# Optimization experiments

Hardware: AMD Instinct MI355X
Metric: run time of the kernel (lower is better)

Reference implementation:

```python
import jax, jax.numpy as jnp
import numpy as np

B, Q, E, NH, L, P = 8, 1024, 256, 8, 4, 4
DH = E // NH
SHAPES = np.array([[128, 128], [64, 64], [32, 32], [16, 16]], dtype=np.int64)
STARTS = np.concatenate([[0], np.cumsum(SHAPES.prod(1))[:-1]]).astype(np.int64)
S_TOTAL = int(SHAPES.prod(1).sum())
EPS = 1e-5


def setup_inputs() -> dict:
    key = jax.random.key(0)
    ks = iter(jax.random.split(key, 40))
    def rn(shp, s=0.02):
        return jax.random.normal(next(ks), shp, jnp.float32) * s
    return {
        "tgt": rn((B, Q, E), 1.0),
        "query_pos": rn((B, Q, E), 1.0),
        "reference_points": jax.random.uniform(next(ks), (B, Q, L, 2), jnp.float32),
        "src": rn((B, S_TOTAL, E), 1.0),
        "spatial_shapes": jnp.asarray(SHAPES),
        "level_start_index": jnp.asarray(STARTS),
        "in_proj_w": rn((3 * E, E)), "in_proj_b": jnp.zeros((3 * E,), jnp.float32),
        "out_proj_w": rn((E, E)), "out_proj_b": jnp.zeros((E,), jnp.float32),
        "norm1_g": jnp.ones((E,), jnp.float32), "norm1_b": jnp.zeros((E,), jnp.float32),
        "off_w": rn((NH * L * P * 2, E)), "off_b": rn((NH * L * P * 2,), 0.5),
        "aw_w": rn((NH * L * P, E)), "aw_b": jnp.zeros((NH * L * P,), jnp.float32),
        "vp_w": rn((E, E)), "vp_b": jnp.zeros((E,), jnp.float32),
        "op_w": rn((E, E)), "op_b": jnp.zeros((E,), jnp.float32),
        "norm2_g": jnp.ones((E,), jnp.float32), "norm2_b": jnp.zeros((E,), jnp.float32),
        "w1": rn((4 * E, E)), "b1": jnp.zeros((4 * E,), jnp.float32),
        "w2": rn((E, 4 * E)), "b2": jnp.zeros((E,), jnp.float32),
        "norm3_g": jnp.ones((E,), jnp.float32), "norm3_b": jnp.zeros((E,), jnp.float32),
    }


def _ln(x, g, b):
    mu = x.mean(-1, keepdims=True)
    var = ((x - mu) ** 2).mean(-1, keepdims=True)
    return (x - mu) * jax.lax.rsqrt(var + EPS) * g + b


def _bilinear(v, loc, Hl, Wl):
    # v: [B,NH,S_l,DH], loc in [0,1]: [B,NH,Q,P,2] -> [B,NH,Q,P,DH]
    # matches torch grid_sample(align_corners=False, padding='zeros')
    x = loc[..., 0] * Wl - 0.5
    y = loc[..., 1] * Hl - 0.5
    x0 = jnp.floor(x)
    y0 = jnp.floor(y)
    wx = (x - x0)[..., None]
    wy = (y - y0)[..., None]
    def g(yi, xi):
        valid = ((xi >= 0) & (xi <= Wl - 1) & (yi >= 0) & (yi <= Hl - 1)).astype(v.dtype)
        idx = (jnp.clip(yi, 0, Hl - 1) * Wl + jnp.clip(xi, 0, Wl - 1)).astype(jnp.int32)
        out = jnp.take_along_axis(v, idx.reshape(B, NH, Q * P, 1), axis=2)
        return out.reshape(B, NH, Q, P, DH) * valid[..., None]
    v00 = g(y0, x0); v01 = g(y0, x0 + 1.0)
    v10 = g(y0 + 1.0, x0); v11 = g(y0 + 1.0, x0 + 1.0)
    return (v00 * (1 - wy) * (1 - wx) + v01 * (1 - wy) * wx
            + v10 * wy * (1 - wx) + v11 * wy * wx)


def _forward(tgt, query_pos, reference_points, src,
             in_proj_w, in_proj_b, out_proj_w, out_proj_b, norm1_g, norm1_b,
             off_w, off_b, aw_w, aw_b, vp_w, vp_b, op_w, op_b,
             norm2_g, norm2_b, w1, b1, w2, b2, norm3_g, norm3_b,
             spatial_shapes, level_start_index):
    shp = np.asarray(spatial_shapes)
    starts = np.asarray(level_start_index)
    # ---- self-attention (q = k = tgt + pos, v = tgt) ----
    qk = tgt + query_pos
    wq, wk, wv = jnp.split(in_proj_w, 3, axis=0)
    bq, bk, bv = jnp.split(in_proj_b, 3, axis=0)
    q = (qk @ wq.T + bq).reshape(B, Q, NH, DH)
    k = (qk @ wk.T + bk).reshape(B, Q, NH, DH)
    v = (tgt @ wv.T + bv).reshape(B, Q, NH, DH)
    scores = jnp.einsum("bqhd,bkhd->bhqk", q, k) / jnp.sqrt(jnp.float32(DH))
    attn = jax.nn.softmax(scores, axis=-1)
    ctx = jnp.einsum("bhqk,bkhd->bqhd", attn, v).reshape(B, Q, E)
    tgt = _ln(tgt + (ctx @ out_proj_w.T + out_proj_b), norm1_g, norm1_b)
    # ---- MSDA cross-attention ----
    query = tgt + query_pos
    value = (src @ vp_w.T + vp_b).reshape(B, S_TOTAL, NH, DH).transpose(0, 2, 1, 3)  # [B,NH,S,DH]
    off = (query @ off_w.T + off_b).reshape(B, Q, NH, L, P, 2)
    aw = jax.nn.softmax((query @ aw_w.T + aw_b).reshape(B, Q, NH, L * P), -1)
    aw = aw.reshape(B, Q, NH, L, P)
    normalizer = jnp.asarray(shp[:, ::-1].copy(), jnp.float32)  # [L,2] = (W,H)
    loc = reference_points[:, :, None, :, None, :] + off / normalizer[None, None, None, :, None, :]
    loc = jnp.transpose(loc, (0, 2, 1, 3, 4, 5))  # [B,NH,Q,L,P,2]
    awt = jnp.transpose(aw, (0, 2, 1, 3, 4))      # [B,NH,Q,L,P]
    out = jnp.zeros((B, NH, Q, DH), jnp.float32)
    for l in range(L):
        Hl, Wl = int(shp[l, 0]), int(shp[l, 1])
        s0 = int(starts[l])
        vl = value[:, :, s0:s0 + Hl * Wl]
        samp = _bilinear(vl, loc[:, :, :, l], Hl, Wl)         # [B,NH,Q,P,DH]
        out = out + (samp * awt[:, :, :, l, :, None]).sum(3)
    ca = out.transpose(0, 2, 1, 3).reshape(B, Q, E) @ op_w.T + op_b
    tgt = _ln(tgt + ca, norm2_g, norm2_b)
    # ---- FFN ----
    h = jax.nn.relu(tgt @ w1.T + b1) @ w2.T + b2
    return _ln(tgt + h, norm3_g, norm3_b)


def reference(tgt, query_pos, reference_points, src, spatial_shapes, level_start_index,
              in_proj_w, in_proj_b, out_proj_w, out_proj_b, norm1_g, norm1_b,
              off_w, off_b, aw_w, aw_b, vp_w, vp_b, op_w, op_b,
              norm2_g, norm2_b, w1, b1, w2, b2, norm3_g, norm3_b):
    return _forward(tgt, query_pos, reference_points, src,
                    in_proj_w, in_proj_b, out_proj_w, out_proj_b, norm1_g, norm1_b,
                    off_w, off_b, aw_w, aw_b, vp_w, vp_b, op_w, op_b,
                    norm2_g, norm2_b, w1, b1, w2, b2, norm3_g, norm3_b,
                    spatial_shapes, level_start_index)
```

## Files before the change

kernel.cpp:

```cpp
#include <hip/hip_runtime.h>
#include <hip/hip_bf16.h>
#include <math.h>

typedef __hip_bfloat16 bf16;
typedef unsigned short ushort_t;

#define BQ 8
#define QLEN 1024
#define EMB 256
#define NHD 8
#define NLVL 4
#define NPT 4
#define DHD 32
#define STOT 21760

typedef short s8v __attribute__((ext_vector_type(8)));
typedef float f4v __attribute__((ext_vector_type(4)));

__device__ __forceinline__ float b2f(bf16 x) { return __bfloat162float(x); }

__device__ __forceinline__ float ldin(const void* p, int bf, size_t i) {
    return bf ? __bfloat162float(((const bf16*)p)[i]) : ((const float*)p)[i];
}

__device__ __forceinline__ float bfraw(unsigned u) {
    union { unsigned i; float f; } c; c.i = u << 16; return c.f;
}

__device__ __forceinline__ unsigned short f2us(float x) {
    bf16 h = __float2bfloat16(x);
    unsigned short u;
    __builtin_memcpy(&u, &h, 2);
    return u;
}

__device__ __forceinline__ void ld4(const void* p, int bf, size_t i, float* o) {
    if (bf) {
        const uint2 u = *(const uint2*)((const ushort_t*)p + i);
        o[0] = bfraw(u.x & 0xffffu); o[1] = bfraw(u.x >> 16);
        o[2] = bfraw(u.y & 0xffffu); o[3] = bfraw(u.y >> 16);
    } else {
        const float4 f = *(const float4*)((const float*)p + i);
        o[0] = f.x; o[1] = f.y; o[2] = f.z; o[3] = f.w;
    }
}

typedef const __attribute__((address_space(1))) unsigned int* gas1_u32;
typedef __attribute__((address_space(3))) unsigned int* las3_u32;
__device__ __forceinline__ void gload_lds16(const void* g, void* l) {
    __builtin_amdgcn_global_load_lds((gas1_u32)g, (las3_u32)l, 16, 0, 0);
}

__global__ void detect_dtype(const unsigned* __restrict__ n1g, int* __restrict__ flag) {
    if (threadIdx.x == 0) flag[0] = (n1g[0] == 0x3F800000u) ? 0 : 1;
}

template <int BN, int KT, bool ARAW, bool RELU, typename CT>
__global__ __launch_bounds__(512) void gemm_wlds(
        const void* __restrict__ A,
        const void* __restrict__ W, int w0,
        const void* __restrict__ bias, int b0,
        CT* __restrict__ C,
        int M, int N,
        const int* __restrict__ dflag) {
    constexpr int GPR = KT / 8;
    constexpr int WSLOTS = BN * GPR;
    constexpr int NJ = BN / 16;
    constexpr int KC = KT / 256;
    constexpr int EPI_ST = BN + 8;
    constexpr int EPI_US = 8 * 16 * EPI_ST * ((int)sizeof(CT) / 2);
    constexpr int SMEM_US = (BN * KT) > EPI_US ? (BN * KT) : EPI_US;

    __shared__ __align__(16) ushort_t smem[SMEM_US];

    const int bfm = *dflag;
    const int tid = threadIdx.x;
    const int lane = tid & 63;
    const int wv = tid >> 6;
    const int l15 = lane & 15, lhi = lane >> 4;
    const int n0 = blockIdx.x * BN;
    const int mg = blockIdx.y * 128 + wv * 16;

#pragma unroll
    for (int i = 0; i < WSLOTS / 512; ++i) {
        const int s = tid + 512 * i;
        const int s0 = (wv << 6) + 512 * i;
        const int n = s / GPR;
        const int gs = s % GPR;
        const int gg = gs ^ (n & 7);
        const size_t woff = (size_t)(w0 + n0 + n) * KT + gg * 8;
        if (bfm) {
            gload_lds16((const ushort_t*)W + woff, smem + (size_t)s0 * 8);
        } else {
            const float* wf = (const float*)W + woff;
            const float4 f0 = *(const float4*)wf;
            const float4 f1 = *(const float4*)(wf + 4);
            ushort_t t[8] = {f2us(f0.x), f2us(f0.y), f2us(f0.z), f2us(f0.w),
                             f2us(f1.x), f2us(f1.y), f2us(f1.z), f2us(f1.w)};
            *(uint4*)(smem + (size_t)s * 8) = *(uint4*)t;
        }
    }

    auto ldA = [&](int kc, s8v* af) {
#pragma unroll
        for (int kk = 0; kk < 8; ++kk) {
            const size_t ao = (size_t)(mg + l15) * KT + kc * 256 + kk * 32 + lhi * 8;
            if (!ARAW || bfm) {
                af[kk] = *(const s8v*)((const ushort_t*)A + ao);
            } else {
                const float* ap = (const float*)A + ao;
                const float4 f0 = *(const float4*)ap;
                const float4 f1 = *(const float4*)(ap + 4);
                ushort_t t[8] = {f2us(f0.x), f2us(f0.y), f2us(f0.z), f2us(f0.w),
                                 f2us(f1.x), f2us(f1.y), f2us(f1.z), f2us(f1.w)};
                af[kk] = *(const s8v*)t;
            }
        }
    };

    f4v acc[NJ] = {};
    s8v afA[8], afB[8];
    ldA(0, afA);
    __syncthreads();

#pragma unroll
    for (int kc = 0; kc < KC; ++kc) {
        s8v* af = (kc & 1) ? afB : afA;
        s8v* afn = (kc & 1) ? afA : afB;
        if (kc + 1 < KC) ldA(kc + 1, afn);
#pragma unroll
        for (int j = 0; j < NJ; ++j) {
            const int n = j * 16 + l15;
#pragma unroll
            for (int kk = 0; kk < 8; ++kk) {
                const int g = ((kc * 8 + kk) * 4 + lhi) ^ (n & 7);
                const s8v b = *(const s8v*)(smem + (size_t)n * KT + g * 8);
                acc[j] = __builtin_amdgcn_mfma_f32_16x16x32_bf16(af[kk], b, acc[j], 0, 0, 0);
            }
        }
    }
    __syncthreads();

    if constexpr (sizeof(CT) == 2) {
        ushort_t* eb = smem + wv * 16 * EPI_ST;
#pragma unroll
        for (int j = 0; j < NJ; ++j) {
            const float bv = ldin(bias, bfm, b0 + n0 + j * 16 + l15);
#pragma unroll
            for (int p = 0; p < 4; ++p) {
                float v = acc[j][p] + bv;
                if (RELU) v = fmaxf(v, 0.f);
                eb[(lhi * 4 + p) * EPI_ST + j * 16 + l15] = f2us(v);
            }
        }
        asm volatile("s_waitcnt lgkmcnt(0)" ::: "memory");
        __builtin_amdgcn_sched_barrier(0);
        constexpr int GPRow = BN / 8;
        constexpr int RPP = 64 / GPRow;
#pragma unroll
        for (int pass = 0; pass < 16 / RPP; ++pass) {
            const int row = pass * RPP + lane / GPRow;
            const int g = lane % GPRow;
            const uint4 u = *(const uint4*)(eb + row * EPI_ST + g * 8);
            *(uint4*)((ushort_t*)C + (size_t)(mg + row) * N + n0 + g * 8) = u;
        }
    } else {
        float* ef = (float*)smem + wv * 16 * EPI_ST;
#pragma unroll
        for (int j = 0; j < NJ; ++j) {
            const float bv = ldin(bias, bfm, b0 + n0 + j * 16 + l15);
#pragma unroll
            for (int p = 0; p < 4; ++p) {
                float v = acc[j][p] + bv;
                if (RELU) v = fmaxf(v, 0.f);
                ef[(lhi * 4 + p) * EPI_ST + j * 16 + l15] = v;
            }
        }
        asm volatile("s_waitcnt lgkmcnt(0)" ::: "memory");
        __builtin_amdgcn_sched_barrier(0);
        constexpr int GPRow = BN / 4;
        constexpr int RPP = 64 / GPRow;
#pragma unroll
        for (int pass = 0; pass < 16 / RPP; ++pass) {
            const int row = pass * RPP + lane / GPRow;
            const int g = lane % GPRow;
            const float4 u = *(const float4*)(ef + row * EPI_ST + g * 4);
            *(float4*)((float*)C + (size_t)(mg + row) * N + n0 + g * 4) = u;
        }
    }
}

__global__ void ew_add_bf(const void* __restrict__ a, const void* __restrict__ b,
                          ushort_t* __restrict__ c, int n4, const int* __restrict__ dflag) {
    const int bfm = *dflag;
    const int i = blockIdx.x * 256 + threadIdx.x;
    if (i < n4) {
        float ta[4], tb[4];
        ld4(a, bfm, (size_t)i * 4, ta);
        ld4(b, bfm, (size_t)i * 4, tb);
        uint2 u;
        u.x = (unsigned)f2us(ta[0] + tb[0]) | ((unsigned)f2us(ta[1] + tb[1]) << 16);
        u.y = (unsigned)f2us(ta[2] + tb[2]) | ((unsigned)f2us(ta[3] + tb[3]) << 16);
        *(uint2*)(c + (size_t)i * 4) = u;
    }
}

__global__ __launch_bounds__(256) void attn_mfma(const ushort_t* __restrict__ qkbuf,
                                                 const ushort_t* __restrict__ v,
                                                 ushort_t* __restrict__ ctx) {
    __shared__ ushort_t Ks[64][40];
    __shared__ ushort_t Vt[32][72];
    __shared__ ushort_t Ps[4][16][72];
    const int bh = blockIdx.y;
    const int b = bh >> 3, h = bh & 7;
    const int qt = blockIdx.x;
    const int tid = threadIdx.x;
    const int lane = tid & 63;
    const int wv = tid >> 6;
    const int l15 = lane & 15, quad = lane >> 4;
    const float scale = 0.17677669529663689f;

    const int qbase = (qt << 6) + (wv << 4);
    const s8v qfrag = *(const s8v*)(qkbuf +
        ((size_t)(b * QLEN + qbase + l15)) * 512 + h * DHD + quad * 8);

    const int sk = tid >> 2;
    const int sd = (tid & 3) << 3;

    float m_run[4] = {-1e30f, -1e30f, -1e30f, -1e30f};
    float l_run[4] = {};
    f4v o[2] = {};

    for (int kt = 0; kt < 16; ++kt) {
        __syncthreads();
        const size_t krow = (size_t)(b * QLEN + (kt << 6) + sk);
        *(uint4*)&Ks[sk][sd] = *(const uint4*)(qkbuf + krow * 512 + 256 + h * DHD + sd);
        const uint4 uv = *(const uint4*)(v + krow * 256 + h * DHD + sd);
        ushort_t vt[8];
        *(uint4*)vt = uv;
#pragma unroll
        for (int j = 0; j < 8; ++j) Vt[sd + j][sk] = vt[j];
        __syncthreads();

        f4v s4[4];
#pragma unroll
        for (int kb = 0; kb < 4; ++kb) {
            const s8v kfr = *(const s8v*)&Ks[(kb << 4) + l15][quad * 8];
            s4[kb] = __builtin_amdgcn_mfma_f32_16x16x32_bf16(qfrag, kfr, f4v{}, 0, 0, 0);
        }

        float sc[4][4];
#pragma unroll
        for (int kb = 0; kb < 4; ++kb)
#pragma unroll
            for (int p = 0; p < 4; ++p) sc[kb][p] = s4[kb][p] * scale;
        float mp[4];
#pragma unroll
        for (int p = 0; p < 4; ++p)
            mp[p] = fmaxf(fmaxf(sc[0][p], sc[1][p]), fmaxf(sc[2][p], sc[3][p]));
#pragma unroll
        for (int p = 0; p < 4; ++p) {
            mp[p] = fmaxf(mp[p], __shfl_xor(mp[p], 1, 64));
            mp[p] = fmaxf(mp[p], __shfl_xor(mp[p], 2, 64));
            mp[p] = fmaxf(mp[p], __shfl_xor(mp[p], 4, 64));
            mp[p] = fmaxf(mp[p], __shfl_xor(mp[p], 8, 64));
        }
        float al[4], ls[4] = {};
#pragma unroll
        for (int p = 0; p < 4; ++p) {
            const float mn = fmaxf(m_run[p], mp[p]);
            al[p] = __expf(m_run[p] - mn);
            m_run[p] = mn;
        }
        float pe[4][4];
#pragma unroll
        for (int kb = 0; kb < 4; ++kb)
#pragma unroll
            for (int p = 0; p < 4; ++p) {
                const float e = __expf(sc[kb][p] - m_run[p]);
                pe[kb][p] = e;
                ls[p] += e;
            }
#pragma unroll
        for (int p = 0; p < 4; ++p) {
            ls[p] += __shfl_xor(ls[p], 1, 64);
            ls[p] += __shfl_xor(ls[p], 2, 64);
            ls[p] += __shfl_xor(ls[p], 4, 64);
            ls[p] += __shfl_xor(ls[p], 8, 64);
            l_run[p] = l_run[p] * al[p] + ls[p];
        }
#pragma unroll
        for (int nb = 0; nb < 2; ++nb)
#pragma unroll
            for (int p = 0; p < 4; ++p) o[nb][p] *= al[p];

#pragma unroll
        for (int kb = 0; kb < 4; ++kb)
#pragma unroll
            for (int p = 0; p < 4; ++p)
                Ps[wv][(quad << 2) + p][(kb << 4) + l15] = f2us(pe[kb][p]);

#pragma unroll
        for (int kk = 0; kk < 2; ++kk) {
            const s8v afr = *(const s8v*)&Ps[wv][l15][kk * 32 + quad * 8];
#pragma unroll
            for (int nb = 0; nb < 2; ++nb) {
                const s8v bfr = *(const s8v*)&Vt[nb * 16 + l15][kk * 32 + quad * 8];
                o[nb] = __builtin_amdgcn_mfma_f32_16x16x32_bf16(afr, bfr, o[nb], 0, 0, 0);
            }
        }
    }

#pragma unroll
    for (int p = 0; p < 4; ++p) {
        const float inv = 1.f / l_run[p];
        const size_t row = (size_t)(b * QLEN + qbase + (quad << 2) + p) * EMB + h * DHD;
#pragma unroll
        for (int nb = 0; nb < 2; ++nb)
            ctx[row + nb * 16 + l15] = f2us(o[nb][p] * inv);
    }
}

__global__ __launch_bounds__(256) void ln_kernel(const void* __restrict__ xb,
                                                 const float* __restrict__ xf1,
                                                 const float* __restrict__ xf2,
                                                 const void* __restrict__ g,
                                                 const void* __restrict__ bta,
                                                 float* __restrict__ out_f,
                                                 ushort_t* __restrict__ out_b,
                                                 void* __restrict__ out_d,
                                                 const void* __restrict__ qp,
                                                 ushort_t* __restrict__ out_q,
                                                 const int* __restrict__ dflag) {
    const int bf = *dflag;
    const int row = blockIdx.x * 4 + (threadIdx.x >> 6);
    const int lane = threadIdx.x & 63;
    const size_t base = (size_t)row * EMB + lane * 4;

    float x[4] = {0.f, 0.f, 0.f, 0.f};
    if (xb) {
        float t[4]; ld4(xb, bf, base, t);
#pragma unroll
        for (int j = 0; j < 4; ++j) x[j] += t[j];
    }
    if (xf1) {
        const float4 f = *(const float4*)(xf1 + base);
        x[0] += f.x; x[1] += f.y; x[2] += f.z; x[3] += f.w;
    }
    if (xf2) {
        const float4 f = *(const float4*)(xf2 + base);
        x[0] += f.x; x[1] += f.y; x[2] += f.z; x[3] += f.w;
    }
    float s = x[0] + x[1] + x[2] + x[3];
#pragma unroll
    for (int o = 1; o < 64; o <<= 1) s += __shfl_xor(s, o, 64);
    const float mu = s * (1.f / EMB);
    float dx[4], vs = 0.f;
#pragma unroll
    for (int j = 0; j < 4; ++j) { dx[j] = x[j] - mu; vs += dx[j] * dx[j]; }
#pragma unroll
    for (int o = 1; o < 64; o <<= 1) vs += __shfl_xor(vs, o, 64);
    const float inv = rsqrtf(vs * (1.f / EMB) + 1e-5f);

    float gv[4], bv[4];
    ld4(g, bf, (size_t)lane * 4, gv);
    ld4(bta, bf, (size_t)lane * 4, bv);
    float y[4];
#pragma unroll
    for (int j = 0; j < 4; ++j) y[j] = dx[j] * inv * gv[j] + bv[j];

    if (out_f) *(float4*)(out_f + base) = float4{y[0], y[1], y[2], y[3]};
    if (out_b) {
        uint2 u;
        u.x = (unsigned)f2us(y[0]) | ((unsigned)f2us(y[1]) << 16);
        u.y = (unsigned)f2us(y[2]) | ((unsigned)f2us(y[3]) << 16);
        *(uint2*)(out_b + base) = u;
    }
    if (out_d) {
        if (bf) {
            uint2 u;
            u.x = (unsigned)f2us(y[0]) | ((unsigned)f2us(y[1]) << 16);
            u.y = (unsigned)f2us(y[2]) | ((unsigned)f2us(y[3]) << 16);
            *(uint2*)((ushort_t*)out_d + base) = u;
        } else {
            *(float4*)((float*)out_d + base) = float4{y[0], y[1], y[2], y[3]};
        }
    }
    if (out_q) {
        float q[4]; ld4(qp, bf, base, q);
        uint2 u;
        u.x = (unsigned)f2us(y[0] + q[0]) | ((unsigned)f2us(y[1] + q[1]) << 16);
        u.y = (unsigned)f2us(y[2] + q[2]) | ((unsigned)f2us(y[3] + q[3]) << 16);
        *(uint2*)(out_q + base) = u;
    }
}

__global__ __launch_bounds__(64) void sample_kernel(const float* __restrict__ offb,
                                                    const float* __restrict__ awb,
                                                    const void* __restrict__ refp,
                                                    const ushort_t* __restrict__ value,
                                                    ushort_t* __restrict__ out,
                                                    const int* __restrict__ dflag) {
    const int bf = *dflag;
    const int bid = blockIdx.x;
    const int h = bid & 7;
    const int bq = bid >> 3;
    const int b = bq >> 10;
    const int lane = threadIdx.x;
    const int s_idx = lane >> 2;
    const int dg = lane & 3;
    const int l = s_idx >> 2;

    float logit = awb[(size_t)bq * 128 + h * 16 + s_idx];
    float m = logit;
#pragma unroll
    for (int o = 32; o > 0; o >>= 1) m = fmaxf(m, __shfl_xor(m, o, 64));
    float e = __expf(logit - m);
    float ssum = e;
#pragma unroll
    for (int o = 32; o > 0; o >>= 1) ssum += __shfl_xor(ssum, o, 64);
    const float paw = 4.f * e / ssum;

    const int Wi = 128 >> l;
    const float Wl = (float)Wi, Hl = (float)Wi;
    const int s0 = (l == 0) ? 0 : (l == 1) ? 16384 : (l == 2) ? 20480 : 21504;

    const float rx = ldin(refp, bf, ((size_t)bq * NLVL + l) * 2 + 0);
    const float ry = ldin(refp, bf, ((size_t)bq * NLVL + l) * 2 + 1);
    const float ox = offb[(size_t)bq * 256 + h * 32 + s_idx * 2 + 0];
    const float oy = offb[(size_t)bq * 256 + h * 32 + s_idx * 2 + 1];
    const float x = (rx + ox / Wl) * Wl - 0.5f;
    const float y = (ry + oy / Hl) * Hl - 0.5f;
    const float x0 = floorf(x), y0 = floorf(y);
    const float wx = x - x0, wy = y - y0;

    float acc[8] = {};
    const ushort_t* vbase = value + ((size_t)b * STOT) * EMB + h * DHD + dg * 8;

    auto corner = [&](float yi, float xi, float w) {
        const bool valid = (xi >= 0.f) && (xi <= Wl - 1.f) && (yi >= 0.f) && (yi <= Hl - 1.f);
        const float xc = fminf(fmaxf(xi, 0.f), Wl - 1.f);
        const float yc = fminf(fmaxf(yi, 0.f), Hl - 1.f);
        const int row = s0 + (int)yc * Wi + (int)xc;
        const uint4 u = *(const uint4*)(vbase + (size_t)row * EMB);
        const float wv = valid ? w : 0.f;
        const unsigned ua[4] = {u.x, u.y, u.z, u.w};
#pragma unroll
        for (int j = 0; j < 4; ++j) {
            acc[2 * j + 0] = fmaf(wv, bfraw(ua[j] & 0xffffu), acc[2 * j + 0]);
            acc[2 * j + 1] = fmaf(wv, bfraw(ua[j] >> 16), acc[2 * j + 1]);
        }
    };
    corner(y0, x0, (1.f - wy) * (1.f - wx));
    corner(y0, x0 + 1.f, (1.f - wy) * wx);
    corner(y0 + 1.f, x0, wy * (1.f - wx));
    corner(y0 + 1.f, x0 + 1.f, wy * wx);

#pragma unroll
    for (int j = 0; j < 8; ++j) {
        float vj = acc[j] * paw;
        vj += __shfl_xor(vj, 4, 64);
        vj += __shfl_xor(vj, 8, 64);
        vj += __shfl_xor(vj, 16, 64);
        vj += __shfl_xor(vj, 32, 64);
        acc[j] = vj;
    }
    if (s_idx == 0) {
        ushort_t t[8];
#pragma unroll
        for (int j = 0; j < 8; ++j) t[j] = f2us(acc[j]);
        *(uint4*)(out + (size_t)bq * EMB + h * DHD + dg * 8) = *(uint4*)t;
    }
}

extern "C" void kernel_launch(void* const* d_in, const int* in_sizes, int n_in,
                              void* d_out, int out_size, void* d_ws, size_t ws_size,
                              hipStream_t stream) {
    const void* tgt  = d_in[0];
    const void* qp   = d_in[1];
    const void* refp = d_in[2];
    const void* src  = d_in[3];
    const void* ipw  = d_in[6];
    const void* ipb  = d_in[7];
    const void* oprw = d_in[8];
    const void* oprb = d_in[9];
    const void* n1g  = d_in[10];
    const void* n1b  = d_in[11];
    const void* ofw  = d_in[12];
    const void* ofb  = d_in[13];
    const void* aww  = d_in[14];
    const void* awbv = d_in[15];
    const void* vpw  = d_in[16];
    const void* vpb  = d_in[17];
    const void* opw2 = d_in[18];
    const void* opb2 = d_in[19];
    const void* n2g  = d_in[20];
    const void* n2b  = d_in[21];
    const void* w1   = d_in[22];
    const void* b1   = d_in[23];
    const void* w2   = d_in[24];
    const void* b2   = d_in[25];
    const void* n3g  = d_in[26];
    const void* n3b  = d_in[27];

    const int M = BQ * QLEN;
    const int MS = BQ * STOT;

    char* ws = (char*)d_ws;
    int* dflag = (int*)ws;
    size_t o = 256;
    char* S1 = ws + o; o += (size_t)M * EMB * 2;
    char* S2 = ws + o; o += (size_t)M * 512 * 2;
    char* S3 = ws + o; o += (size_t)M * EMB * 2;
    char* S4 = ws + o; o += (size_t)M * EMB * 2;
    char* S5 = ws + o; o += (size_t)M * EMB * 4;
    char* S6 = ws + o; o += (size_t)M * EMB * 4;
    char* S7 = ws + o; o += (size_t)M * EMB * 4;
    char* S8 = ws + o;

    ushort_t* qk_bf    = (ushort_t*)S1;
    ushort_t* samp_bf  = (ushort_t*)S1;
    ushort_t* qkproj   = (ushort_t*)S2;
    float*    off_f    = (float*)S2;
    ushort_t* vproj    = (ushort_t*)S3;
    ushort_t* qry_bf   = (ushort_t*)S3;
    ushort_t* tgt2_bf  = (ushort_t*)S3;
    ushort_t* ctx_bf   = (ushort_t*)S4;
    float*    awl_f    = (float*)S4;
    float*    bufD     = (float*)S5;
    float*    tgt1_f   = (float*)S6;
    float*    tgt2_f   = (float*)S7;
    ushort_t* value_bf = (ushort_t*)S8;
    ushort_t* h1_bf    = (ushort_t*)S8;

    detect_dtype<<<1, 64, 0, stream>>>((const unsigned*)n1g, dflag);

    ew_add_bf<<<(M * EMB / 4) / 256, 256, 0, stream>>>(tgt, qp, qk_bf, M * EMB / 4, dflag);
    gemm_wlds<256, 256, false, false, ushort_t><<<dim3(2, M / 128), 512, 0, stream>>>(
        qk_bf, ipw, 0, ipb, 0, qkproj, M, 512, dflag);
    gemm_wlds<256, 256, true, false, ushort_t><<<dim3(1, M / 128), 512, 0, stream>>>(
        tgt, ipw, 512, ipb, 512, vproj, M, 256, dflag);
    attn_mfma<<<dim3(16, BQ * NHD), 256, 0, stream>>>(qkproj, vproj, ctx_bf);
    gemm_wlds<256, 256, false, false, float><<<dim3(1, M / 128), 512, 0, stream>>>(
        ctx_bf, oprw, 0, oprb, 0, bufD, M, 256, dflag);
    ln_kernel<<<M / 4, 256, 0, stream>>>(tgt, bufD, nullptr, n1g, n1b,
                                         tgt1_f, nullptr, nullptr, qp, qry_bf, dflag);

    gemm_wlds<256, 256, false, false, float><<<dim3(1, M / 128), 512, 0, stream>>>(
        qry_bf, ofw, 0, ofb, 0, off_f, M, 256, dflag);
    gemm_wlds<128, 256, false, false, float><<<dim3(1, M / 128), 512, 0, stream>>>(
        qry_bf, aww, 0, awbv, 0, awl_f, M, 128, dflag);
    gemm_wlds<256, 256, true, false, ushort_t><<<dim3(1, MS / 128), 512, 0, stream>>>(
        src, vpw, 0, vpb, 0, value_bf, MS, 256, dflag);
    sample_kernel<<<M * NHD, 64, 0, stream>>>(off_f, awl_f, refp, value_bf, samp_bf, dflag);
    gemm_wlds<256, 256, false, false, float><<<dim3(1, M / 128), 512, 0, stream>>>(
        samp_bf, opw2, 0, opb2, 0, bufD, M, 256, dflag);
    ln_kernel<<<M / 4, 256, 0, stream>>>(nullptr, tgt1_f, bufD, n2g, n2b,
                                         tgt2_f, tgt2_bf, nullptr, nullptr, nullptr, dflag);

    gemm_wlds<256, 256, false, true, ushort_t><<<dim3(4, M / 128), 512, 0, stream>>>(
        tgt2_bf, w1, 0, b1, 0, h1_bf, M, 1024, dflag);
    gemm_wlds<64, 1024, false, false, float><<<dim3(4, M / 128), 512, 0, stream>>>(
        h1_bf, w2, 0, b2, 0, bufD, M, 256, dflag);
    ln_kernel<<<M / 4, 256, 0, stream>>>(nullptr, tgt2_f, bufD, n3g, n3b,
                                         nullptr, nullptr, d_out, nullptr, nullptr, dflag);
}
```

Baseline: 667.5 us.

## Parameterize GEMM wave count, shrink tiles, rotate LDS swizzle, chunk epilogue

The weight-in-LDS GEMM now takes a wave count as a template parameter, and most projection GEMMs switch to narrow 64-column, 4-wave blocks. This launches many more, smaller blocks so the 8192-row GEMMs fill more of the GPU's compute units. The large value projection instead uses 16 waves and 256 rows per block. The LDS swizzle changes from XOR to a rotation modulo the group count, so it stays valid for narrow K/BN tiles. The epilogue is staged in 128-column chunks to cap LDS use. In exchange, each weight tile is reloaded by more blocks, and the 1024-thread blocks may limit occupancy.

```diff
diff --git a/kernel.cpp b/kernel.cpp
--- a/kernel.cpp
+++ b/kernel.cpp
@@ -55,20 +55,24 @@
     if (threadIdx.x == 0) flag[0] = (n1g[0] == 0x3F800000u) ? 0 : 1;
 }
 
-template <int BN, int KT, bool ARAW, bool RELU, typename CT>
-__global__ __launch_bounds__(512) void gemm_wlds(
+template <int BN, int KT, int WAVES, bool ARAW, bool RELU, typename CT>
+__global__ __launch_bounds__(WAVES * 64) void gemm_wlds(
         const void* __restrict__ A,
         const void* __restrict__ W, int w0,
         const void* __restrict__ bias, int b0,
         CT* __restrict__ C,
         int M, int N,
         const int* __restrict__ dflag) {
+    constexpr int T = WAVES * 64;
     constexpr int GPR = KT / 8;
     constexpr int WSLOTS = BN * GPR;
     constexpr int NJ = BN / 16;
     constexpr int KC = KT / 256;
-    constexpr int EPI_ST = BN + 8;
-    constexpr int EPI_US = 8 * 16 * EPI_ST * ((int)sizeof(CT) / 2);
+    constexpr int CW = BN < 128 ? BN : 128;
+    constexpr int NCH = BN / CW;
+    constexpr int JC = CW / 16;
+    constexpr int ST_US = (sizeof(CT) == 2) ? (CW + 8) : 2 * (CW + 12);
+    constexpr int EPI_US = WAVES * 16 * ST_US;
     constexpr int SMEM_US = (BN * KT) > EPI_US ? (BN * KT) : EPI_US;
 
     __shared__ __align__(16) ushort_t smem[SMEM_US];
@@ -79,15 +83,15 @@
     const int wv = tid >> 6;
     const int l15 = lane & 15, lhi = lane >> 4;
     const int n0 = blockIdx.x * BN;
-    const int mg = blockIdx.y * 128 + wv * 16;
-
-#pragma unroll
-    for (int i = 0; i < WSLOTS / 512; ++i) {
-        const int s = tid + 512 * i;
-        const int s0 = (wv << 6) + 512 * i;
+    const int mg = blockIdx.y * (16 * WAVES) + wv * 16;
+
+#pragma unroll
+    for (int i = 0; i < WSLOTS / T; ++i) {
+        const int s0 = (wv << 6) + T * i;
+        const int s = s0 + lane;
         const int n = s / GPR;
-        const int gs = s % GPR;
-        const int gg = gs ^ (n & 7);
+        const int gl = s & (GPR - 1);
+        const int gg = (gl + GPR - (n & (GPR - 1))) & (GPR - 1);
         const size_t woff = (size_t)(w0 + n0 + n) * KT + gg * 8;
         if (bfm) {
             gload_lds16((const ushort_t*)W + woff, smem + (size_t)s0 * 8);
@@ -133,8 +137,9 @@
             const int n = j * 16 + l15;
 #pragma unroll
             for (int kk = 0; kk < 8; ++kk) {
-                const int g = ((kc * 8 + kk) * 4 + lhi) ^ (n & 7);
-                const s8v b = *(const s8v*)(smem + (size_t)n * KT + g * 8);
+                const int gg = kc * 32 + kk * 4 + lhi;
+                const int gl = (gg + n) & (GPR - 1);
+                const s8v b = *(const s8v*)(smem + (size_t)n * KT + gl * 8);
                 acc[j] = __builtin_amdgcn_mfma_f32_16x16x32_bf16(af[kk], b, acc[j], 0, 0, 0);
             }
         }
@@ -142,50 +147,63 @@
     __syncthreads();
 
     if constexpr (sizeof(CT) == 2) {
-        ushort_t* eb = smem + wv * 16 * EPI_ST;
-#pragma unroll
-        for (int j = 0; j < NJ; ++j) {
-            const float bv = ldin(bias, bfm, b0 + n0 + j * 16 + l15);
-#pragma unroll
-            for (int p = 0; p < 4; ++p) {
-                float v = acc[j][p] + bv;
-                if (RELU) v = fmaxf(v, 0.f);
-                eb[(lhi * 4 + p) * EPI_ST + j * 16 + l15] = f2us(v);
-            }
-        }
-        asm volatile("s_waitcnt lgkmcnt(0)" ::: "memory");
-        __builtin_amdgcn_sched_barrier(0);
-        constexpr int GPRow = BN / 8;
-        constexpr int RPP = 64 / GPRow;
-#pragma unroll
-        for (int pass = 0; pass < 16 / RPP; ++pass) {
-            const int row = pass * RPP + lane / GPRow;
-            const int g = lane % GPRow;
-            const uint4 u = *(const uint4*)(eb + row * EPI_ST + g * 8);
-            *(uint4*)((ushort_t*)C + (size_t)(mg + row) * N + n0 + g * 8) = u;
+        ushort_t* eb = smem + wv * 16 * ST_US;
+#pragma unroll
+        for (int c = 0; c < NCH; ++c) {
+#pragma unroll
+            for (int jj = 0; jj < JC; ++jj) {
+                const int j = c * JC + jj;
+                const float bv = ldin(bias, bfm, b0 + n0 + j * 16 + l15);
+#pragma unroll
+                for (int p = 0; p < 4; ++p) {
+                    float v = acc[j][p] + bv;
+                    if (RELU) v = fmaxf(v, 0.f);
+                    eb[(lhi * 4 + p) * ST_US + jj * 16 + l15] = f2us(v);
+                }
+            }
+            asm volatile("s_waitcnt lgkmcnt(0)" ::: "memory");
+            __builtin_amdgcn_sched_barrier(0);
+            constexpr int GPRow = CW / 8;
+            constexpr int RPP = 64 / GPRow;
+#pragma unroll
+            for (int pass = 0; pass < 16 / RPP; ++pass) {
+                const int row = pass * RPP + lane / GPRow;
+                const int g = lane % GPRow;
+                const uint4 u = *(const uint4*)(eb + row * ST_US + g * 8);
+                *(uint4*)((ushort_t*)C + (size_t)(mg + row) * N + n0 + c * CW + g * 8) = u;
+            }
+            asm volatile("s_waitcnt lgkmcnt(0)" ::: "memory");
+            __builtin_amdgcn_sched_barrier(0);
         }
     } else {
-        float* ef = (float*)smem + wv * 16 * EPI_ST;
-#pragma unroll
-        for (int j = 0; j < NJ; ++j) {
-            const float bv = ldin(bias, bfm, b0 + n0 + j * 16 + l15);
-#pragma unroll
-            for (int p = 0; p < 4; ++p) {
-                float v = acc[j][p] + bv;
-                if (RELU) v = fmaxf(v, 0.f);
-                ef[(lhi * 4 + p) * EPI_ST + j * 16 + l15] = v;
-            }
-        }
-        asm volatile("s_waitcnt lgkmcnt(0)" ::: "memory");
-        __builtin_amdgcn_sched_barrier(0);
-        constexpr int GPRow = BN / 4;
-        constexpr int RPP = 64 / GPRow;
-#pragma unroll
-        for (int pass = 0; pass < 16 / RPP; ++pass) {
-            const int row = pass * RPP + lane / GPRow;
-            const int g = lane % GPRow;
-            const float4 u = *(const float4*)(ef + row * EPI_ST + g * 4);
-            *(float4*)((float*)C + (size_t)(mg + row) * N + n0 + g * 4) = u;
+        constexpr int ST_F = CW + 12;
+        float* ef = (float*)(smem) + wv * 16 * ST_F;
+#pragma unroll
+        for (int c = 0; c < NCH; ++c) {
+#pragma unroll
+            for (int jj = 0; jj < JC; ++jj) {
+                const int j = c * JC + jj;
+                const float bv = ldin(bias, bfm, b0 + n0 + j * 16 + l15);
+#pragma unroll
+                for (int p = 0; p < 4; ++p) {
+                    float v = acc[j][p] + bv;
+                    if (RELU) v = fmaxf(v, 0.f);
+                    ef[(lhi * 4 + p) * ST_F + jj * 16 + l15] = v;
+                }
+            }
+            asm volatile("s_waitcnt lgkmcnt(0)" ::: "memory");
+            __builtin_amdgcn_sched_barrier(0);
+            constexpr int GPRow = CW / 4;
+            constexpr int RPP = 64 / GPRow;
+#pragma unroll
+            for (int pass = 0; pass < 16 / RPP; ++pass) {
+                const int row = pass * RPP + lane / GPRow;
+                const int g = lane % GPRow;
+                const float4 u = *(const float4*)(ef + row * ST_F + g * 4);
+                *(float4*)((float*)C + (size_t)(mg + row) * N + n0 + c * CW + g * 4) = u;
+            }
+            asm volatile("s_waitcnt lgkmcnt(0)" ::: "memory");
+            __builtin_amdgcn_sched_barrier(0);
         }
     }
 }
@@ -536,31 +554,31 @@
     detect_dtype<<<1, 64, 0, stream>>>((const unsigned*)n1g, dflag);
 
     ew_add_bf<<<(M * EMB / 4) / 256, 256, 0, stream>>>(tgt, qp, qk_bf, M * EMB / 4, dflag);
-    gemm_wlds<256, 256, false, false, ushort_t><<<dim3(2, M / 128), 512, 0, stream>>>(
+    gemm_wlds<64, 256, 4, false, false, ushort_t><<<dim3(8, M / 64), 256, 0, stream>>>(
         qk_bf, ipw, 0, ipb, 0, qkproj, M, 512, dflag);
-    gemm_wlds<256, 256, true, false, ushort_t><<<dim3(1, M / 128), 512, 0, stream>>>(
+    gemm_wlds<64, 256, 4, true, false, ushort_t><<<dim3(4, M / 64), 256, 0, stream>>>(
         tgt, ipw, 512, ipb, 512, vproj, M, 256, dflag);
     attn_mfma<<<dim3(16, BQ * NHD), 256, 0, stream>>>(qkproj, vproj, ctx_bf);
-    gemm_wlds<256, 256, false, false, float><<<dim3(1, M / 128), 512, 0, stream>>>(
+    gemm_wlds<64, 256, 4, false, false, float><<<dim3(4, M / 64), 256, 0, stream>>>(
         ctx_bf, oprw, 0, oprb, 0, bufD, M, 256, dflag);
     ln_kernel<<<M / 4, 256, 0, stream>>>(tgt, bufD, nullptr, n1g, n1b,
                                          tgt1_f, nullptr, nullptr, qp, qry_bf, dflag);
 
-    gemm_wlds<256, 256, false, false, float><<<dim3(1, M / 128), 512, 0, stream>>>(
+    gemm_wlds<64, 256, 4, false, false, float><<<dim3(4, M / 64), 256, 0, stream>>>(
         qry_bf, ofw, 0, ofb, 0, off_f, M, 256, dflag);
-    gemm_wlds<128, 256, false, false, float><<<dim3(1, M / 128), 512, 0, stream>>>(
+    gemm_wlds<64, 256, 4, false, false, float><<<dim3(2, M / 64), 256, 0, stream>>>(
         qry_bf, aww, 0, awbv, 0, awl_f, M, 128, dflag);
-    gemm_wlds<256, 256, true, false, ushort_t><<<dim3(1, MS / 128), 512, 0, stream>>>(
+    gemm_wlds<256, 256, 16, true, false, ushort_t><<<dim3(1, MS / 256), 1024, 0, stream>>>(
         src, vpw, 0, vpb, 0, value_bf, MS, 256, dflag);
     sample_kernel<<<M * NHD, 64, 0, stream>>>(off_f, awl_f, refp, value_bf, samp_bf, dflag);
-    gemm_wlds<256, 256, false, false, float><<<dim3(1, M / 128), 512, 0, stream>>>(
+    gemm_wlds<64, 256, 4, false, false, float><<<dim3(4, M / 64), 256, 0, stream>>>(
         samp_bf, opw2, 0, opb2, 0, bufD, M, 256, dflag);
     ln_kernel<<<M / 4, 256, 0, stream>>>(nullptr, tgt1_f, bufD, n2g, n2b,
                                          tgt2_f, tgt2_bf, nullptr, nullptr, nullptr, dflag);
 
-    gemm_wlds<256, 256, false, true, ushort_t><<<dim3(4, M / 128), 512, 0, stream>>>(
+    gemm_wlds<64, 256, 4, false, true, ushort_t><<<dim3(16, M / 64), 256, 0, stream>>>(
         tgt2_bf, w1, 0, b1, 0, h1_bf, M, 1024, dflag);
-    gemm_wlds<64, 1024, false, false, float><<<dim3(4, M / 128), 512, 0, stream>>>(
+    gemm_wlds<32, 1024, 4, false, false, float><<<dim3(8, M / 64), 256, 0, stream>>>(
         h1_bf, w2, 0, b2, 0, bufD, M, 256, dflag);
     ln_kernel<<<M / 4, 256, 0, stream>>>(nullptr, tgt2_f, bufD, n3g, n3b,
                                          nullptr, nullptr, d_out, nullptr, nullptr, dflag);
```

Result: faster. 596.5 us (-10.6%).
